# Kernel optimization log

Measured on AMD Instinct MI355X. Metric: run time of the kernel, lower is better.

The kernel has to match this reference:

```python
import jax, jax.numpy as jnp
import numpy as np


def setup_inputs() -> dict:
    key = jax.random.key(0)
    k1, k2 = jax.random.split(key)
    B, C_in, H, Wd = 8, 64, 64, 64
    C_a = 32
    x = jax.random.normal(k1, (B, C_in, H, Wd), dtype=jnp.float32)
    # 1x1 conv == per-pixel linear map: weight [C_a, C_in], bias [C_a]
    W = jax.random.normal(k2, (C_a, C_in), dtype=jnp.float32) * (1.0 / np.sqrt(C_in))
    b = jnp.zeros((C_a,), dtype=jnp.float32)
    return {"x": x, "W": W, "b": b}


def reference(x, W, b):
    B, C, H, Wd = x.shape
    N = H * Wd
    # g = 1x1 conv: [B, C_a, H, W] -> flatten spatial -> [B, C_a, N]
    g = jnp.einsum('oc,bchw->bohw', W, x) + b[None, :, None, None]
    g = g.reshape(B, -1, N)
    # alpha[b, n, m] = softmax_m( sum_c g[b,c,n] * g[b,c,m] )  (unscaled)
    scores = jnp.einsum('bcn,bcm->bnm', g, g)
    alpha = jax.nn.softmax(scores, axis=2)
    # r[b, c, n] = sum_m alpha[b,n,m] * x[b,c,m]
    xf = x.reshape(B, C, N)
    r = jnp.einsum('bnm,bcm->bcn', alpha, xf)
    # residual (intended semantics of is_residual=True) + ReLU epilogue
    r = r + xf
    out = jax.nn.relu(r).reshape(B, C, H, Wd)
    return (out, alpha)
```

## Files before the change

### kernel.cpp

```cpp
#include <hip/hip_runtime.h>
#include <math.h>

#define BB 8
#define CC 64
#define NA 4096
#define KA 32
#define RB 32

typedef short bfrag __attribute__((ext_vector_type(8)));
typedef int   i4    __attribute__((ext_vector_type(4)));
typedef float f4    __attribute__((ext_vector_type(4)));
typedef float f16v  __attribute__((ext_vector_type(16)));

__device__ __forceinline__ f16v mf(bfrag a, bfrag b, f16v c) {
    return __builtin_amdgcn_mfma_f32_32x32x16_bf16(a, b, c, 0, 0, 0);
}

__device__ __forceinline__ unsigned short bfrne(float f) {
    unsigned u = __builtin_bit_cast(unsigned, f);
    return (unsigned short)((u + 0x7FFFu + ((u >> 16) & 1u)) >> 16);
}
__device__ __forceinline__ unsigned pk2(float a, float b) {
    return (unsigned)bfrne(a) | ((unsigned)bfrne(b) << 16);
}
__device__ __forceinline__ float bf2f(unsigned short h) {
    unsigned u = ((unsigned)h) << 16;
    return __builtin_bit_cast(float, u);
}

__global__ __launch_bounds__(256) void k_g(const float* __restrict__ x,
                                           const float* __restrict__ W,
                                           const float* __restrict__ bias,
                                           short* __restrict__ ghi,
                                           short* __restrict__ glo,
                                           float* __restrict__ norms) {
    __shared__ float Wl[KA * CC];
    __shared__ float bl[KA];
    int tid = threadIdx.x;
    for (int i = tid; i < KA * CC; i += 256) Wl[i] = W[i];
    if (tid < KA) bl[tid] = bias[tid];
    __syncthreads();

    int b = blockIdx.y;
    int n = blockIdx.x * 256 + tid;

    float acc[KA];
#pragma unroll
    for (int k = 0; k < KA; k++) acc[k] = 0.f;

    const float* xp = x + (size_t)b * CC * NA + n;
#pragma unroll 4
    for (int c = 0; c < CC; c++) {
        float xv = xp[(size_t)c * NA];
#pragma unroll
        for (int k = 0; k < KA; k++) acc[k] = fmaf(Wl[k * CC + c], xv, acc[k]);
    }

    float ss = 0.f;
    unsigned ph[KA / 2], pl[KA / 2];
#pragma unroll
    for (int k = 0; k < KA; k += 2) {
        float v0 = acc[k] + bl[k];
        float v1 = acc[k + 1] + bl[k + 1];
        ss = fmaf(v0, v0, fmaf(v1, v1, ss));
        unsigned short h0 = bfrne(v0), h1 = bfrne(v1);
        float l0 = v0 - bf2f(h0), l1 = v1 - bf2f(h1);
        ph[k / 2] = (unsigned)h0 | ((unsigned)h1 << 16);
        pl[k / 2] = (unsigned)bfrne(l0) | ((unsigned)bfrne(l1) << 16);
    }
    norms[b * NA + n] = sqrtf(ss);

    size_t row = ((size_t)b * NA + n) * KA;
#pragma unroll
    for (int q = 0; q < 4; q++) {
        i4 vh = { (int)ph[4 * q], (int)ph[4 * q + 1], (int)ph[4 * q + 2], (int)ph[4 * q + 3] };
        i4 vl = { (int)pl[4 * q], (int)pl[4 * q + 1], (int)pl[4 * q + 2], (int)pl[4 * q + 3] };
        *(i4*)(ghi + row + q * 8) = vh;
        *(i4*)(glo + row + q * 8) = vl;
    }
}

__global__ __launch_bounds__(256) void k_gmax(const float* __restrict__ norms,
                                              float* __restrict__ gmaxp) {
    int b = blockIdx.x, tid = threadIdx.x;
    float m = 0.f;
    for (int i = tid; i < NA; i += 256) m = fmaxf(m, norms[b * NA + i]);
#pragma unroll
    for (int off = 1; off < 64; off <<= 1) m = fmaxf(m, __shfl_xor(m, off));
    __shared__ float red[4];
    if ((tid & 63) == 0) red[tid >> 6] = m;
    __syncthreads();
    if (tid == 0) gmaxp[b] = fmaxf(fmaxf(red[0], red[1]), fmaxf(red[2], red[3]));
}

__global__ __launch_bounds__(256) void k_xb(const float* __restrict__ x,
                                            short* __restrict__ xb) {
    size_t idx = ((size_t)blockIdx.x * 256 + threadIdx.x) * 4;
    f4 v = *(const f4*)(x + idx);
    int2 p;
    p.x = (int)pk2(v[0], v[1]);
    p.y = (int)pk2(v[2], v[3]);
    *(int2*)(xb + idx) = p;
}

__global__ __launch_bounds__(256, 3) void k_attn(const float* __restrict__ x,
                                                 const short* __restrict__ ghi,
                                                 const short* __restrict__ glo,
                                                 const short* __restrict__ xb,
                                                 const float* __restrict__ norms,
                                                 const float* __restrict__ gmaxp,
                                                 float* __restrict__ out,
                                                 float* __restrict__ alpha) {
    __shared__ __align__(16) float astage[RB][128];
    __shared__ float rowsum[4][RB];
    __shared__ float pvred[2][RB][CC + 1];

    const int tid = threadIdx.x;
    const int w = tid >> 6;
    const int l = tid & 63;
    const int l31 = l & 31;
    const int hi = l >> 5;
    const int b = blockIdx.y;
    const int n0 = blockIdx.x * RB;

    const float M = norms[b * NA + n0 + l31] * gmaxp[b];

    const short* gh = ghi + (size_t)b * NA * KA;
    const short* gl = glo + (size_t)b * NA * KA;

    bfrag Bh[2], Bl[2];
#pragma unroll
    for (int kt = 0; kt < 2; kt++) {
        size_t o = (size_t)(n0 + l31) * KA + kt * 16 + hi * 8;
        Bh[kt] = *(const bfrag*)(gh + o);
        Bl[kt] = *(const bfrag*)(gl + o);
    }

    float ls = 0.f;
    for (int i = 0; i < 32; i++) {
        const int m0 = i * 128 + w * 32;
        bfrag Ah[2], Al[2];
#pragma unroll
        for (int kt = 0; kt < 2; kt++) {
            size_t o = (size_t)(m0 + l31) * KA + kt * 16 + hi * 8;
            Ah[kt] = *(const bfrag*)(gh + o);
            Al[kt] = *(const bfrag*)(gl + o);
        }
        f16v s = {};
#pragma unroll
        for (int kt = 0; kt < 2; kt++) {
            s = mf(Ah[kt], Bh[kt], s);
            s = mf(Ah[kt], Bl[kt], s);
            s = mf(Al[kt], Bh[kt], s);
        }
#pragma unroll
        for (int r = 0; r < 16; r++) ls += __expf(s[r] - M);
    }
    ls += __shfl_xor(ls, 32);
    if (hi == 0) rowsum[w][l31] = ls;
    __syncthreads();
    const float L = 1.f / (rowsum[0][l31] + rowsum[1][l31] + rowsum[2][l31] + rowsum[3][l31]);

    f16v pv0 = {}, pv1 = {};
    const short* xp = xb + (size_t)b * CC * NA;
    float* ap = alpha + (size_t)b * NA * NA;

    for (int i = 0; i < 32; i++) {
        const int m0 = i * 128 + w * 32;
        bfrag Ah[2], Al[2];
#pragma unroll
        for (int kt = 0; kt < 2; kt++) {
            size_t o = (size_t)(m0 + l31) * KA + kt * 16 + hi * 8;
            Ah[kt] = *(const bfrag*)(gh + o);
            Al[kt] = *(const bfrag*)(gl + o);
        }
        f16v s = {};
#pragma unroll
        for (int kt = 0; kt < 2; kt++) {
            s = mf(Ah[kt], Bh[kt], s);
            s = mf(Ah[kt], Bl[kt], s);
            s = mf(Al[kt], Bh[kt], s);
        }

        float a[16];
#pragma unroll
        for (int r = 0; r < 16; r++) a[r] = __expf(s[r] - M) * L;

#pragma unroll
        for (int q = 0; q < 4; q++) {
            f4 v = { a[4 * q], a[4 * q + 1], a[4 * q + 2], a[4 * q + 3] };
            int clog = w * 8 + 2 * q + hi;
            int phys = clog ^ (l31 & 7);
            *(f4*)&astage[l31][phys * 4] = v;
        }

        unsigned p0 = pk2(a[0], a[1]),   p1 = pk2(a[2], a[3]);
        unsigned p2 = pk2(a[4], a[5]),   p3 = pk2(a[6], a[7]);
        unsigned p4 = pk2(a[8], a[9]),   p5 = pk2(a[10], a[11]);
        unsigned p6 = pk2(a[12], a[13]), p7 = pk2(a[14], a[15]);
        asm("v_permlane32_swap_b32 %0, %1" : "+v"(p0), "+v"(p2));
        asm("v_permlane32_swap_b32 %0, %1" : "+v"(p1), "+v"(p3));
        asm("v_permlane32_swap_b32 %0, %1" : "+v"(p4), "+v"(p6));
        asm("v_permlane32_swap_b32 %0, %1" : "+v"(p5), "+v"(p7));
        i4 f0 = { (int)p0, (int)p1, (int)p2, (int)p3 };
        i4 f1 = { (int)p4, (int)p5, (int)p6, (int)p7 };
        bfrag pa0 = __builtin_bit_cast(bfrag, f0);
        bfrag pa1 = __builtin_bit_cast(bfrag, f1);

        size_t ox0 = (size_t)l31 * NA + m0 + hi * 8;
        size_t ox1 = (size_t)(32 + l31) * NA + m0 + hi * 8;
        bfrag X00 = *(const bfrag*)(xp + ox0);
        bfrag X01 = *(const bfrag*)(xp + ox0 + 16);
        bfrag X10 = *(const bfrag*)(xp + ox1);
        bfrag X11 = *(const bfrag*)(xp + ox1 + 16);

        pv0 = mf(pa0, X00, pv0); pv0 = mf(pa1, X01, pv0);
        pv1 = mf(pa0, X10, pv1); pv1 = mf(pa1, X11, pv1);

        __syncthreads();
#pragma unroll
        for (int e = 0; e < 4; e++) {
            int row = e * 8 + (tid >> 5);
            int clog = tid & 31;
            int phys = clog ^ (row & 7);
            f4 v = *(const f4*)&astage[row][phys * 4];
            *(f4*)(ap + (size_t)(n0 + row) * NA + i * 128 + clog * 4) = v;
        }
        __syncthreads();
    }

    if (w >= 2) {
        float (*buf)[CC + 1] = pvred[w - 2];
#pragma unroll
        for (int r = 0; r < 16; r++) {
            int nl = (r & 3) + 8 * (r >> 2) + 4 * hi;
            buf[nl][l31]      = pv0[r];
            buf[nl][32 + l31] = pv1[r];
        }
    }
    __syncthreads();
    if (w < 2) {
        float (*buf)[CC + 1] = pvred[w];
#pragma unroll
        for (int r = 0; r < 16; r++) {
            int nl = (r & 3) + 8 * (r >> 2) + 4 * hi;
            buf[nl][l31]      += pv0[r];
            buf[nl][32 + l31] += pv1[r];
        }
    }
    __syncthreads();

    const float* xr = x + (size_t)b * CC * NA + n0;
    float* op = out + (size_t)b * CC * NA + n0;
#pragma unroll
    for (int e = 0; e < 8; e++) {
        int idx = e * 256 + tid;
        int c = idx >> 5, n = idx & 31;
        float v = pvred[0][n][c] + pvred[1][n][c] + xr[(size_t)c * NA + n];
        op[(size_t)c * NA + n] = fmaxf(v, 0.f);
    }
}

extern "C" void kernel_launch(void* const* d_in, const int* in_sizes, int n_in,
                              void* d_out, int out_size, void* d_ws, size_t ws_size,
                              hipStream_t stream) {
    const float* x = (const float*)d_in[0];
    const float* W = (const float*)d_in[1];
    const float* bias = (const float*)d_in[2];

    float* out = (float*)d_out;
    float* alpha = out + (size_t)BB * CC * NA;

    short* ghi = (short*)d_ws;
    short* glo = ghi + (size_t)BB * NA * KA;
    short* xb  = glo + (size_t)BB * NA * KA;
    float* norms = (float*)(xb + (size_t)BB * CC * NA);
    float* gmaxp = norms + (size_t)BB * NA;

    k_g<<<dim3(NA / 256, BB), 256, 0, stream>>>(x, W, bias, ghi, glo, norms);
    k_gmax<<<BB, 256, 0, stream>>>(norms, gmaxp);
    k_xb<<<(BB * CC * NA) / (256 * 4), 256, 0, stream>>>(x, xb);
    k_attn<<<dim3(NA / RB, BB), 256, 0, stream>>>(x, ghi, glo, xb, norms, gmaxp, out, alpha);
}
```

Baseline: 224.8 us.

## Split softmax denominator into parallel kernel and pipeline x tiles through LDS

The row-sum pass is moved out of the attention kernel into a separate kernel that splits the m dimension four ways across more blocks, followed by a small reduction kernel that writes the inverse sums. The attention kernel then runs a single pass: it prefetches the next g fragments and double-buffers bf16 x tiles through LDS, which replaces direct strided global loads. It also uses exp2 with a folded log2e FMA, separates the hi and lo MFMA accumulators, and interleaves batches in the block index. The aim is more parallelism for the denominator pass and overlap of loads with compute, at the cost of extra launches and a little extra workspace traffic.

```diff
diff --git a/kernel.cpp b/kernel.cpp
--- a/kernel.cpp
+++ b/kernel.cpp
@@ -5,7 +5,7 @@
 #define CC 64
 #define NA 4096
 #define KA 32
-#define RB 32
+#define LOG2E 1.4426950408889634f
 
 typedef short bfrag __attribute__((ext_vector_type(8)));
 typedef int   i4    __attribute__((ext_vector_type(4)));
@@ -103,28 +103,24 @@
     *(int2*)(xb + idx) = p;
 }
 
-__global__ __launch_bounds__(256, 3) void k_attn(const float* __restrict__ x,
-                                                 const short* __restrict__ ghi,
-                                                 const short* __restrict__ glo,
-                                                 const short* __restrict__ xb,
-                                                 const float* __restrict__ norms,
-                                                 const float* __restrict__ gmaxp,
-                                                 float* __restrict__ out,
-                                                 float* __restrict__ alpha) {
-    __shared__ __align__(16) float astage[RB][128];
-    __shared__ float rowsum[4][RB];
-    __shared__ float pvred[2][RB][CC + 1];
-
+__global__ __launch_bounds__(256, 4) void k_den(const short* __restrict__ ghi,
+                                                const short* __restrict__ glo,
+                                                const float* __restrict__ norms,
+                                                const float* __restrict__ gmaxp,
+                                                float* __restrict__ partial) {
+    __shared__ float rowsum[4][32];
     const int tid = threadIdx.x;
     const int w = tid >> 6;
-    const int l = tid & 63;
-    const int l31 = l & 31;
-    const int hi = l >> 5;
-    const int b = blockIdx.y;
-    const int n0 = blockIdx.x * RB;
-
-    const float M = norms[b * NA + n0 + l31] * gmaxp[b];
-
+    const int l31 = tid & 31;
+    const int hi = (tid >> 5) & 1;
+    const int id = blockIdx.x;
+    const int b = id & 7;
+    const int rr = id >> 3;
+    const int nb = rr & 127;
+    const int mc = rr >> 7;
+    const int n0 = nb * 32;
+
+    const float C2 = -norms[b * NA + n0 + l31] * gmaxp[b] * LOG2E;
     const short* gh = ghi + (size_t)b * NA * KA;
     const short* gl = glo + (size_t)b * NA * KA;
 
@@ -137,8 +133,9 @@
     }
 
     float ls = 0.f;
-    for (int i = 0; i < 32; i++) {
-        const int m0 = i * 128 + w * 32;
+#pragma unroll 2
+    for (int i = 0; i < 8; i++) {
+        const int m0 = (mc * 8 + i) * 128 + w * 32;
         bfrag Ah[2], Al[2];
 #pragma unroll
         for (int kt = 0; kt < 2; kt++) {
@@ -146,52 +143,125 @@
             Ah[kt] = *(const bfrag*)(gh + o);
             Al[kt] = *(const bfrag*)(gl + o);
         }
-        f16v s = {};
-#pragma unroll
-        for (int kt = 0; kt < 2; kt++) {
-            s = mf(Ah[kt], Bh[kt], s);
-            s = mf(Ah[kt], Bl[kt], s);
-            s = mf(Al[kt], Bh[kt], s);
-        }
-#pragma unroll
-        for (int r = 0; r < 16; r++) ls += __expf(s[r] - M);
+        f16v sA = {}, sB = {};
+        sA = mf(Ah[0], Bh[0], sA); sA = mf(Ah[1], Bh[1], sA);
+        sB = mf(Ah[0], Bl[0], sB); sB = mf(Ah[1], Bl[1], sB);
+        sB = mf(Al[0], Bh[0], sB); sB = mf(Al[1], Bh[1], sB);
+#pragma unroll
+        for (int r = 0; r < 16; r++) ls += exp2f(fmaf(sA[r] + sB[r], LOG2E, C2));
     }
     ls += __shfl_xor(ls, 32);
     if (hi == 0) rowsum[w][l31] = ls;
     __syncthreads();
-    const float L = 1.f / (rowsum[0][l31] + rowsum[1][l31] + rowsum[2][l31] + rowsum[3][l31]);
-
-    f16v pv0 = {}, pv1 = {};
+    if (tid < 32)
+        partial[((size_t)mc * BB + b) * NA + n0 + tid] =
+            rowsum[0][tid] + rowsum[1][tid] + rowsum[2][tid] + rowsum[3][tid];
+}
+
+__global__ __launch_bounds__(256) void k_red(const float* __restrict__ partial,
+                                             float* __restrict__ linv) {
+    int i = blockIdx.x * 256 + threadIdx.x;
+    const size_t S = (size_t)BB * NA;
+    linv[i] = 1.f / (partial[i] + partial[S + i] + partial[2 * S + i] + partial[3 * S + i]);
+}
+
+__global__ __launch_bounds__(256, 3) void k_attn2(const float* __restrict__ x,
+                                                  const short* __restrict__ ghi,
+                                                  const short* __restrict__ glo,
+                                                  const short* __restrict__ xb,
+                                                  const float* __restrict__ norms,
+                                                  const float* __restrict__ gmaxp,
+                                                  const float* __restrict__ linv,
+                                                  float* __restrict__ out,
+                                                  float* __restrict__ alpha) {
+    __shared__ __align__(16) char smem[34816 + 16384];
+    short* xt = (short*)smem;
+    float* ast = (float*)(smem + 34816);
+
+    const int tid = threadIdx.x;
+    const int w = tid >> 6;
+    const int l31 = tid & 31;
+    const int hi = (tid >> 5) & 1;
+    const int id = blockIdx.x;
+    const int b = id & 7;
+    const int n0 = (id >> 3) * 32;
+
+    const float M = norms[b * NA + n0 + l31] * gmaxp[b];
+    const float C2 = -M * LOG2E;
+    const float L = linv[b * NA + n0 + l31];
+
+    const short* gh = ghi + (size_t)b * NA * KA;
+    const short* gl = glo + (size_t)b * NA * KA;
     const short* xp = xb + (size_t)b * CC * NA;
     float* ap = alpha + (size_t)b * NA * NA;
 
-    for (int i = 0; i < 32; i++) {
-        const int m0 = i * 128 + w * 32;
-        bfrag Ah[2], Al[2];
-#pragma unroll
-        for (int kt = 0; kt < 2; kt++) {
-            size_t o = (size_t)(m0 + l31) * KA + kt * 16 + hi * 8;
-            Ah[kt] = *(const bfrag*)(gh + o);
-            Al[kt] = *(const bfrag*)(gl + o);
-        }
-        f16v s = {};
-#pragma unroll
-        for (int kt = 0; kt < 2; kt++) {
-            s = mf(Ah[kt], Bh[kt], s);
-            s = mf(Ah[kt], Bl[kt], s);
-            s = mf(Al[kt], Bh[kt], s);
-        }
-
+    bfrag Bh[2], Bl[2];
+#pragma unroll
+    for (int kt = 0; kt < 2; kt++) {
+        size_t o = (size_t)(n0 + l31) * KA + kt * 16 + hi * 8;
+        Bh[kt] = *(const bfrag*)(gh + o);
+        Bl[kt] = *(const bfrag*)(gl + o);
+    }
+
+    const int sc = tid >> 2, ss = tid & 3;
+
+    i4 xs[4];
+    {
+        const short* src = xp + (size_t)sc * NA;
+#pragma unroll
+        for (int i = 0; i < 4; i++) xs[i] = *(const i4*)(src + ss * 32 + i * 8);
+    }
+    bfrag Ah[2], Al[2];
+#pragma unroll
+    for (int kt = 0; kt < 2; kt++) {
+        size_t o = (size_t)(w * 32 + l31) * KA + kt * 16 + hi * 8;
+        Ah[kt] = *(const bfrag*)(gh + o);
+        Al[kt] = *(const bfrag*)(gl + o);
+    }
+#pragma unroll
+    for (int i = 0; i < 4; i++) *(i4*)(xt + sc * 136 + ss * 32 + i * 8) = xs[i];
+    __syncthreads();
+
+    f16v pv0 = {}, pv1 = {};
+    int cur = 0;
+
+    for (int it = 0; it < 32; ++it) {
+        if (it < 31) {
+            const short* src = xp + (size_t)sc * NA + (it + 1) * 128;
+#pragma unroll
+            for (int i = 0; i < 4; i++) xs[i] = *(const i4*)(src + ss * 32 + i * 8);
+        }
+        f16v sA = {}, sB = {};
+        sA = mf(Ah[0], Bh[0], sA); sA = mf(Ah[1], Bh[1], sA);
+        sB = mf(Ah[0], Bl[0], sB); sB = mf(Ah[1], Bl[1], sB);
+        sB = mf(Al[0], Bh[0], sB); sB = mf(Al[1], Bh[1], sB);
+        if (it < 31) {
+            const int m0n = (it + 1) * 128 + w * 32;
+#pragma unroll
+            for (int kt = 0; kt < 2; kt++) {
+                size_t o = (size_t)(m0n + l31) * KA + kt * 16 + hi * 8;
+                Ah[kt] = *(const bfrag*)(gh + o);
+                Al[kt] = *(const bfrag*)(gl + o);
+            }
+        }
         float a[16];
 #pragma unroll
-        for (int r = 0; r < 16; r++) a[r] = __expf(s[r] - M) * L;
-
+        for (int r = 0; r < 16; r++) a[r] = exp2f(fmaf(sA[r] + sB[r], LOG2E, C2)) * L;
 #pragma unroll
         for (int q = 0; q < 4; q++) {
             f4 v = { a[4 * q], a[4 * q + 1], a[4 * q + 2], a[4 * q + 3] };
-            int clog = w * 8 + 2 * q + hi;
-            int phys = clog ^ (l31 & 7);
-            *(f4*)&astage[l31][phys * 4] = v;
+            int phys = (w * 8 + 2 * q + hi) ^ (l31 & 7);
+            *(f4*)&ast[l31 * 128 + phys * 4] = v;
+        }
+        __syncthreads();
+
+#pragma unroll
+        for (int e = 0; e < 4; e++) {
+            int row = e * 8 + (tid >> 5);
+            int clog = tid & 31;
+            int phys = clog ^ (row & 7);
+            f4 v = *(const f4*)&ast[row * 128 + phys * 4];
+            *(f4*)(ap + (size_t)(n0 + row) * NA + it * 128 + clog * 4) = v;
         }
 
         unsigned p0 = pk2(a[0], a[1]),   p1 = pk2(a[2], a[3]);
@@ -207,30 +277,27 @@
         bfrag pa0 = __builtin_bit_cast(bfrag, f0);
         bfrag pa1 = __builtin_bit_cast(bfrag, f1);
 
-        size_t ox0 = (size_t)l31 * NA + m0 + hi * 8;
-        size_t ox1 = (size_t)(32 + l31) * NA + m0 + hi * 8;
-        bfrag X00 = *(const bfrag*)(xp + ox0);
-        bfrag X01 = *(const bfrag*)(xp + ox0 + 16);
-        bfrag X10 = *(const bfrag*)(xp + ox1);
-        bfrag X11 = *(const bfrag*)(xp + ox1 + 16);
-
+        const short* xc = xt + cur * 8704;
+        bfrag X00 = *(const bfrag*)(xc + l31 * 136 + w * 32 + hi * 8);
+        bfrag X01 = *(const bfrag*)(xc + l31 * 136 + w * 32 + hi * 8 + 16);
         pv0 = mf(pa0, X00, pv0); pv0 = mf(pa1, X01, pv0);
+        bfrag X10 = *(const bfrag*)(xc + (32 + l31) * 136 + w * 32 + hi * 8);
+        bfrag X11 = *(const bfrag*)(xc + (32 + l31) * 136 + w * 32 + hi * 8 + 16);
         pv1 = mf(pa0, X10, pv1); pv1 = mf(pa1, X11, pv1);
 
+        if (it < 31) {
+            short* xn = xt + (cur ^ 1) * 8704;
+#pragma unroll
+            for (int i = 0; i < 4; i++) *(i4*)(xn + sc * 136 + ss * 32 + i * 8) = xs[i];
+        }
         __syncthreads();
-#pragma unroll
-        for (int e = 0; e < 4; e++) {
-            int row = e * 8 + (tid >> 5);
-            int clog = tid & 31;
-            int phys = clog ^ (row & 7);
-            f4 v = *(const f4*)&astage[row][phys * 4];
-            *(f4*)(ap + (size_t)(n0 + row) * NA + i * 128 + clog * 4) = v;
-        }
-        __syncthreads();
-    }
-
+        cur ^= 1;
+    }
+
+    float (*pvr0)[CC + 1] = (float(*)[CC + 1])smem;
+    float (*pvr1)[CC + 1] = (float(*)[CC + 1])(smem + 32 * (CC + 1) * 4);
     if (w >= 2) {
-        float (*buf)[CC + 1] = pvred[w - 2];
+        float (*buf)[CC + 1] = (w == 2) ? pvr0 : pvr1;
 #pragma unroll
         for (int r = 0; r < 16; r++) {
             int nl = (r & 3) + 8 * (r >> 2) + 4 * hi;
@@ -240,7 +307,7 @@
     }
     __syncthreads();
     if (w < 2) {
-        float (*buf)[CC + 1] = pvred[w];
+        float (*buf)[CC + 1] = (w == 0) ? pvr0 : pvr1;
 #pragma unroll
         for (int r = 0; r < 16; r++) {
             int nl = (r & 3) + 8 * (r >> 2) + 4 * hi;
@@ -256,7 +323,7 @@
     for (int e = 0; e < 8; e++) {
         int idx = e * 256 + tid;
         int c = idx >> 5, n = idx & 31;
-        float v = pvred[0][n][c] + pvred[1][n][c] + xr[(size_t)c * NA + n];
+        float v = pvr0[n][c] + pvr1[n][c] + xr[(size_t)c * NA + n];
         op[(size_t)c * NA + n] = fmaxf(v, 0.f);
     }
 }
@@ -276,9 +343,13 @@
     short* xb  = glo + (size_t)BB * NA * KA;
     float* norms = (float*)(xb + (size_t)BB * CC * NA);
     float* gmaxp = norms + (size_t)BB * NA;
+    float* partial = gmaxp + BB;
+    float* linv = partial + (size_t)4 * BB * NA;
 
     k_g<<<dim3(NA / 256, BB), 256, 0, stream>>>(x, W, bias, ghi, glo, norms);
     k_gmax<<<BB, 256, 0, stream>>>(norms, gmaxp);
     k_xb<<<(BB * CC * NA) / (256 * 4), 256, 0, stream>>>(x, xb);
-    k_attn<<<dim3(NA / RB, BB), 256, 0, stream>>>(x, ghi, glo, xb, norms, gmaxp, out, alpha);
-}
+    k_den<<<4096, 256, 0, stream>>>(ghi, glo, norms, gmaxp, partial);
+    k_red<<<BB * NA / 256, 256, 0, stream>>>(partial, linv);
+    k_attn2<<<1024, 256, 0, stream>>>(x, ghi, glo, xb, norms, gmaxp, linv, out, alpha);
+}
```

Result: no change. 222.0 us (-1.3%).
